# Optimization experiments

Hardware: AMD Instinct MI355X
Metric: run time of the kernel (lower is better)

## Reference

```python
import jax, jax.numpy as jnp
import numpy as np

D_MODEL = 2048
N_HEADS = 16
HEAD_DIM = 128
KV_RANK = 512


def setup_inputs() -> dict:
    key = jax.random.key(0)
    ks = jax.random.split(key, 6)
    s = lambda fan_in: 1.0 / np.sqrt(fan_in)
    return {
        "x": jax.random.normal(ks[0], (2, 2048, D_MODEL), dtype=jnp.float32),
        "Wq": jax.random.normal(ks[1], (D_MODEL, N_HEADS * HEAD_DIM), dtype=jnp.float32) * s(D_MODEL),
        "Wdown": jax.random.normal(ks[2], (D_MODEL, KV_RANK), dtype=jnp.float32) * s(D_MODEL),
        "Wk_up": jax.random.normal(ks[3], (KV_RANK, N_HEADS * HEAD_DIM), dtype=jnp.float32) * s(KV_RANK),
        "Wv_up": jax.random.normal(ks[4], (KV_RANK, N_HEADS * HEAD_DIM), dtype=jnp.float32) * s(KV_RANK),
        "Wo": jax.random.normal(ks[5], (N_HEADS * HEAD_DIM, D_MODEL), dtype=jnp.float32) * s(N_HEADS * HEAD_DIM),
    }


def reference(x, Wq, Wdown, Wk_up, Wv_up, Wo):
    B, T, _ = x.shape
    H, Dh = N_HEADS, HEAD_DIM
    # Q projection: (B,T,H,Dh) -> (B,H,T,Dh)
    Q = (x @ Wq).reshape(B, T, H, Dh).transpose(0, 2, 1, 3)
    # latent compression (this is the cached tensor)
    c = x @ Wdown  # (B, T, kv_lora_rank)
    # up-project latent to full K/V heads
    K = (c @ Wk_up).reshape(B, T, H, Dh).transpose(0, 2, 1, 3)
    V = (c @ Wv_up).reshape(B, T, H, Dh).transpose(0, 2, 1, 3)
    # causal SDPA (mask=None, past_kv=None -> is_causal=True), dropout=0
    scale = Dh ** (-0.5)
    scores = jnp.einsum("bhqd,bhkd->bhqk", Q, K) * scale
    causal = jnp.tril(jnp.ones((T, T), dtype=bool))
    scores = jnp.where(causal[None, None], scores, jnp.finfo(scores.dtype).min)
    attn = jax.nn.softmax(scores, axis=-1)
    out = jnp.einsum("bhqk,bhkd->bhqd", attn, V)
    out = out.transpose(0, 2, 1, 3).reshape(B, T, H * Dh)
    return out @ Wo, c
```

## Files before the change

### kernel.cpp

```cpp
#include <hip/hip_runtime.h>

typedef short bf16x8 __attribute__((ext_vector_type(8)));
typedef float f32x4 __attribute__((ext_vector_type(4)));

__device__ __forceinline__ void async16(const void* g, const void* l) {
  __builtin_amdgcn_global_load_lds(
      (const __attribute__((address_space(1))) unsigned int*)g,
      (__attribute__((address_space(3))) unsigned int*)(void*)(uintptr_t)l,
      16, 0, 0);
}

__device__ __forceinline__ unsigned short f2b(float f) {
  unsigned int u = __float_as_uint(f);
  u += 0x7fffu + ((u >> 16) & 1u);
  return (unsigned short)(u >> 16);
}

__global__ __launch_bounds__(256) void cast_f32_bf16(
    const float* __restrict__ in, unsigned short* __restrict__ out, int n) {
  int i = (blockIdx.x * 256 + threadIdx.x) * 4;
  if (i < n) {
    float4 v = *(const float4*)(in + i);
    ushort4 o;
    o.x = f2b(v.x); o.y = f2b(v.y); o.z = f2b(v.z); o.w = f2b(v.w);
    *(ushort4*)(out + i) = o;
  }
}

__global__ __launch_bounds__(256) void transpose_cast(
    const float* __restrict__ in, unsigned short* __restrict__ out,
    int K, int N) {
  __shared__ __align__(16) unsigned short tile[64][65];
  const int k0 = blockIdx.y * 64, n0 = blockIdx.x * 64;
  const int tid = threadIdx.x;
  const int r = tid >> 4, c4 = tid & 15;
#pragma unroll
  for (int p = 0; p < 4; ++p) {
    int row = p * 16 + r;
    float4 v = *(const float4*)(in + (size_t)(k0 + row) * N + n0 + c4 * 4);
    tile[c4 * 4 + 0][row] = f2b(v.x);
    tile[c4 * 4 + 1][row] = f2b(v.y);
    tile[c4 * 4 + 2][row] = f2b(v.z);
    tile[c4 * 4 + 3][row] = f2b(v.w);
  }
  __syncthreads();
#pragma unroll
  for (int p = 0; p < 4; ++p) {
    int nr = p * 16 + r;
    ushort4 o;
    o.x = tile[nr][c4 * 4 + 0];
    o.y = tile[nr][c4 * 4 + 1];
    o.z = tile[nr][c4 * 4 + 2];
    o.w = tile[nr][c4 * 4 + 3];
    *(ushort4*)(out + (size_t)(n0 + nr) * K + k0 + c4 * 4) = o;
  }
}

__global__ __launch_bounds__(256) void gemm_bt(
    const unsigned short* __restrict__ A, const unsigned short* __restrict__ BT,
    unsigned short* __restrict__ Cb, float* __restrict__ Cf, int M, int N, int K,
    float cscale) {
  __shared__ __align__(16) unsigned short sA[128 * 64];
  __shared__ __align__(16) unsigned short sB[128 * 64];
  const int tid = threadIdx.x;
  const int wave = tid >> 6, lane = tid & 63;
  const int quad = lane >> 4, cl = lane & 15;
  const int m0 = blockIdx.y * 128, n0 = blockIdx.x * 128;
  const int wm = (wave >> 1) * 64, wn = (wave & 1) * 64;
  (void)M;

  f32x4 acc[4][4] = {};

  const unsigned short* gA = A + (size_t)(m0 + wave * 32 + (lane >> 3)) * K + (lane & 7) * 8;
  const unsigned short* gB = BT + (size_t)(n0 + wave * 32 + (lane >> 3)) * K + (lane & 7) * 8;
  char* lA = (char*)sA + (wave * 32) * 128;
  char* lB = (char*)sB + (wave * 32) * 128;

  for (int kt = 0; kt < K; kt += 64) {
#pragma unroll
    for (int r = 0; r < 4; ++r) {
      async16(gA + (size_t)r * 8 * K + kt, lA + r * 8 * 128);
      async16(gB + (size_t)r * 8 * K + kt, lB + r * 8 * 128);
    }
    __syncthreads();
#pragma unroll
    for (int kk = 0; kk < 64; kk += 32) {
      bf16x8 af[4], bfr[4];
#pragma unroll
      for (int i = 0; i < 4; ++i)
        af[i] = *(const bf16x8*)((const char*)sA + (wm + i * 16 + cl) * 128 + kk * 2 + quad * 16);
#pragma unroll
      for (int j = 0; j < 4; ++j)
        bfr[j] = *(const bf16x8*)((const char*)sB + (wn + j * 16 + cl) * 128 + kk * 2 + quad * 16);
#pragma unroll
      for (int i = 0; i < 4; ++i)
#pragma unroll
        for (int j = 0; j < 4; ++j)
          acc[i][j] = __builtin_amdgcn_mfma_f32_16x16x32_bf16(af[i], bfr[j], acc[i][j], 0, 0, 0);
    }
    __syncthreads();
  }
#pragma unroll
  for (int i = 0; i < 4; ++i)
#pragma unroll
    for (int j = 0; j < 4; ++j)
#pragma unroll
      for (int r = 0; r < 4; ++r) {
        int row = m0 + wm + i * 16 + quad * 4 + r;
        int col = n0 + wn + j * 16 + cl;
        float v = acc[i][j][r];
        if (Cb) Cb[(size_t)row * N + col] = f2b(v * cscale);
        if (Cf) Cf[(size_t)row * N + col] = v;
      }
}

__global__ __launch_bounds__(256) void gemm_qc(
    const unsigned short* __restrict__ A, const unsigned short* __restrict__ BT,
    unsigned short* __restrict__ Qb, unsigned short* __restrict__ cb,
    float* __restrict__ cout, int K, float qscale) {
  __shared__ __align__(16) unsigned short sA[128 * 64];
  __shared__ __align__(16) unsigned short sB[128 * 64];
  const int tid = threadIdx.x;
  const int wave = tid >> 6, lane = tid & 63;
  const int quad = lane >> 4, cl = lane & 15;
  const int m0 = blockIdx.y * 128, n0 = blockIdx.x * 128;
  const int wm = (wave >> 1) * 64, wn = (wave & 1) * 64;

  f32x4 acc[4][4] = {};

  const unsigned short* gA = A + (size_t)(m0 + wave * 32 + (lane >> 3)) * K + (lane & 7) * 8;
  const unsigned short* gB = BT + (size_t)(n0 + wave * 32 + (lane >> 3)) * K + (lane & 7) * 8;
  char* lA = (char*)sA + (wave * 32) * 128;
  char* lB = (char*)sB + (wave * 32) * 128;

  for (int kt = 0; kt < K; kt += 64) {
#pragma unroll
    for (int r = 0; r < 4; ++r) {
      async16(gA + (size_t)r * 8 * K + kt, lA + r * 8 * 128);
      async16(gB + (size_t)r * 8 * K + kt, lB + r * 8 * 128);
    }
    __syncthreads();
#pragma unroll
    for (int kk = 0; kk < 64; kk += 32) {
      bf16x8 af[4], bfr[4];
#pragma unroll
      for (int i = 0; i < 4; ++i)
        af[i] = *(const bf16x8*)((const char*)sA + (wm + i * 16 + cl) * 128 + kk * 2 + quad * 16);
#pragma unroll
      for (int j = 0; j < 4; ++j)
        bfr[j] = *(const bf16x8*)((const char*)sB + (wn + j * 16 + cl) * 128 + kk * 2 + quad * 16);
#pragma unroll
      for (int i = 0; i < 4; ++i)
#pragma unroll
        for (int j = 0; j < 4; ++j)
          acc[i][j] = __builtin_amdgcn_mfma_f32_16x16x32_bf16(af[i], bfr[j], acc[i][j], 0, 0, 0);
    }
    __syncthreads();
  }
  const bool qreg = (n0 < 2048);
#pragma unroll
  for (int i = 0; i < 4; ++i)
#pragma unroll
    for (int j = 0; j < 4; ++j)
#pragma unroll
      for (int r = 0; r < 4; ++r) {
        int row = m0 + wm + i * 16 + quad * 4 + r;
        int col = n0 + wn + j * 16 + cl;
        float v = acc[i][j][r];
        if (qreg) {
          Qb[(size_t)row * 2048 + col] = f2b(v * qscale);
        } else {
          int c2 = col - 2048;
          cb[(size_t)row * 512 + c2] = f2b(v);
          cout[(size_t)row * 512 + c2] = v;
        }
      }
}

__global__ __launch_bounds__(256) void mla_attn(
    const unsigned short* __restrict__ Qm, const unsigned short* __restrict__ Km,
    const unsigned short* __restrict__ Vt, unsigned short* __restrict__ Om, int T) {
  const int ld = 2048;
  const int ldv = 4096;
  __shared__ __align__(16) unsigned short sK[2][64 * 128];
  __shared__ __align__(16) unsigned short sVT[128 * 64];
  __shared__ __align__(16) unsigned short sP[64 * 64];
  const int h = blockIdx.y, b = blockIdx.z;
  const int tid = threadIdx.x, wave = tid >> 6, lane = tid & 63;
  const int quad = lane >> 4, cl = lane & 15;
  const int nq = T / 64;

  for (int phase = 0; phase < 2; ++phase) {
    const int qt = phase ? (nq - 1 - blockIdx.x) : blockIdx.x;

    bf16x8 qf[4];
    {
      const unsigned short* Qg =
          Qm + (size_t)(b * T + qt * 64 + wave * 16 + cl) * ld + h * 128 + quad * 8;
#pragma unroll
      for (int kk = 0; kk < 4; ++kk)
        qf[kk] = *(const bf16x8*)(Qg + kk * 32);
    }

    float m_i[4], l_part[4];
    f32x4 acc_o[8] = {};
#pragma unroll
    for (int r = 0; r < 4; ++r) { m_i[r] = -1e30f; l_part[r] = 0.f; }

    const unsigned short* Kg0 = Km + (size_t)(b * T) * ld + h * 128;
    const unsigned short* Vg0 = Vt + (size_t)(h * 128) * ldv + (size_t)b * T;

#pragma unroll
    for (int r = 0; r < 4; ++r) {
      int c0 = r * 256 + wave * 64;
      int c = c0 + lane;
      int row = c >> 4, j = (c & 15) ^ (row & 7);
      async16(Kg0 + (size_t)row * ld + j * 8, (char*)sK[0] + c0 * 16);
    }
    __syncthreads();

    for (int kt = 0; kt <= qt; ++kt) {
      const int cur = kt & 1;
      const char* cK = (const char*)sK[cur];

      if (kt < qt) {
        const unsigned short* Kg = Kg0 + (size_t)(kt + 1) * 64 * ld;
        char* dK = (char*)sK[cur ^ 1];
#pragma unroll
        for (int r = 0; r < 4; ++r) {
          int c0 = r * 256 + wave * 64;
          int c = c0 + lane;
          int row = c >> 4, j = (c & 15) ^ (row & 7);
          async16(Kg + (size_t)row * ld + j * 8, dK + c0 * 16);
        }
      }
      {
        const unsigned short* Vg = Vg0 + kt * 64;
#pragma unroll
        for (int r = 0; r < 4; ++r) {
          int c0 = r * 256 + wave * 64;
          int c = c0 + lane;
          int d = c >> 3, jv = (c & 7) ^ (d & 7);
          async16(Vg + (size_t)d * ldv + jv * 8, (char*)sVT + c0 * 16);
        }
      }

      f32x4 s[4] = {};
      __builtin_amdgcn_s_setprio(1);
#pragma unroll
      for (int kk = 0; kk < 4; ++kk) {
#pragma unroll
        for (int j = 0; j < 4; ++j) {
          int t = j * 16 + cl;
          int jp = (kk * 4 + quad) ^ (t & 7);
          bf16x8 bk = *(const bf16x8*)(cK + (t * 16 + jp) * 16);
          s[j] = __builtin_amdgcn_mfma_f32_16x16x32_bf16(qf[kk], bk, s[j], 0, 0, 0);
        }
      }
      __builtin_amdgcn_s_setprio(0);

      const bool need_mask = (kt == qt);
#pragma unroll
      for (int r = 0; r < 4; ++r) {
        int q_l = wave * 16 + quad * 4 + r;
        float mxl = -1e30f;
#pragma unroll
        for (int j = 0; j < 4; ++j) {
          float v = s[j][r];
          if (need_mask) {
            int t_l = j * 16 + cl;
            if (t_l > q_l) v = -1e30f;
            s[j][r] = v;
          }
          mxl = fmaxf(mxl, v);
        }
        if (__any(mxl > m_i[r] + 6.f)) {
          float mx = mxl;
#pragma unroll
          for (int off = 1; off < 16; off <<= 1)
            mx = fmaxf(mx, __shfl_xor(mx, off));
          float m_new = fmaxf(m_i[r], mx);
          float alpha = exp2f(m_i[r] - m_new);
          m_i[r] = m_new;
          l_part[r] *= alpha;
#pragma unroll
          for (int jd = 0; jd < 8; ++jd)
            acc_o[jd][r] *= alpha;
        }
        float rs = 0.f;
#pragma unroll
        for (int j = 0; j < 4; ++j) {
          float p = exp2f(s[j][r] - m_i[r]);
          s[j][r] = p;
          rs += p;
        }
        l_part[r] += rs;
      }

#pragma unroll
      for (int j = 0; j < 4; ++j)
#pragma unroll
        for (int r = 0; r < 4; ++r) {
          int q = wave * 16 + quad * 4 + r;
          int swz = (q & 7) ^ (((q >> 3) & 1) << 1);
          int t = j * 16 + cl;
          int jp = (t >> 3) ^ swz;
          sP[(q * 8 + jp) * 8 + (t & 7)] = f2b(s[j][r]);
        }

      __syncthreads();

      __builtin_amdgcn_s_setprio(1);
#pragma unroll
      for (int kk2 = 0; kk2 < 2; ++kk2) {
        int q = wave * 16 + cl;
        int swz = (q & 7) ^ (((q >> 3) & 1) << 1);
        int jp = (kk2 * 4 + quad) ^ swz;
        bf16x8 ap = *(const bf16x8*)((const char*)sP + (q * 8 + jp) * 16);
#pragma unroll
        for (int jd = 0; jd < 8; ++jd) {
          int d = jd * 16 + cl;
          int jpv = (kk2 * 4 + quad) ^ (d & 7);
          bf16x8 bv = *(const bf16x8*)((const char*)sVT + (d * 8 + jpv) * 16);
          acc_o[jd] = __builtin_amdgcn_mfma_f32_16x16x32_bf16(ap, bv, acc_o[jd], 0, 0, 0);
        }
      }
      __builtin_amdgcn_s_setprio(0);

      __syncthreads();
    }

#pragma unroll
    for (int r = 0; r < 4; ++r) {
      float l = l_part[r];
#pragma unroll
      for (int off = 1; off < 16; off <<= 1)
        l += __shfl_xor(l, off);
      float inv = 1.f / l;
      int row = b * T + qt * 64 + wave * 16 + quad * 4 + r;
#pragma unroll
      for (int jd = 0; jd < 8; ++jd)
        Om[(size_t)row * ld + h * 128 + jd * 16 + cl] = f2b(acc_o[jd][r] * inv);
    }
  }
}

extern "C" void kernel_launch(void* const* d_in, const int* in_sizes, int n_in,
                              void* d_out, int out_size, void* d_ws, size_t ws_size,
                              hipStream_t stream) {
  (void)in_sizes; (void)n_in; (void)out_size; (void)ws_size;
  const int B = 2, T = 2048, Dm = 2048, H = 16, Dh = 128, R = 512;
  const int M = B * T;
  const float* x     = (const float*)d_in[0];
  const float* Wq    = (const float*)d_in[1];
  const float* Wdown = (const float*)d_in[2];
  const float* Wkup  = (const float*)d_in[3];
  const float* Wvup  = (const float*)d_in[4];
  const float* Wo    = (const float*)d_in[5];

  float* out  = (float*)d_out;
  float* cout = out + (size_t)M * Dm;

  unsigned short* ws  = (unsigned short*)d_ws;
  unsigned short* WqT = ws;
  unsigned short* WdT = WqT + (size_t)Dm * Dm;
  unsigned short* WoT = WdT + (size_t)R * Dm;
  unsigned short* WkT = WoT + (size_t)Dm * Dm;
  unsigned short* WvT = WkT + (size_t)Dm * R;
  unsigned short* xb  = WvT + (size_t)Dm * R;
  unsigned short* cb  = xb + (size_t)M * Dm;
  unsigned short* Qb  = cb + (size_t)M * R;
  unsigned short* Kb  = Qb + (size_t)M * Dm;
  unsigned short* VT  = Kb + (size_t)M * Dm;
  unsigned short* AO  = xb;

  const float qscale = 0.08838834764831845f * 1.4426950408889634f;

  cast_f32_bf16<<<(M * Dm) / 1024, 256, 0, stream>>>(x, xb, M * Dm);
  transpose_cast<<<dim3(32, 32), 256, 0, stream>>>(Wq, WqT, Dm, Dm);
  transpose_cast<<<dim3(8, 32), 256, 0, stream>>>(Wdown, WdT, Dm, R);
  transpose_cast<<<dim3(32, 32), 256, 0, stream>>>(Wo, WoT, Dm, Dm);
  transpose_cast<<<dim3(32, 8), 256, 0, stream>>>(Wkup, WkT, R, Dm);
  transpose_cast<<<dim3(32, 8), 256, 0, stream>>>(Wvup, WvT, R, Dm);

  gemm_qc<<<dim3(20, 32), 256, 0, stream>>>(xb, WqT, Qb, cb, cout, Dm, qscale);

  gemm_bt<<<dim3(Dm / 128, M / 128), 256, 0, stream>>>(cb, WkT, Kb, nullptr, M, Dm, R, 1.f);
  gemm_bt<<<dim3(M / 128, Dm / 128), 256, 0, stream>>>(WvT, cb, VT, nullptr, Dm, M, R, 1.f);

  mla_attn<<<dim3(T / 128, H, B), 256, 0, stream>>>(Qb, Kb, VT, AO, T);

  gemm_bt<<<dim3(Dm / 128, M / 128), 256, 0, stream>>>(AO, WoT, nullptr, out, M, Dm, Dm, 1.f);
  (void)Dh; (void)H;
}
```

Measured before the change: 398.7 us.

## Double-buffer LDS tiles and XOR-swizzle layout in projection GEMMs

Both projection GEMM kernels (gemm_bt and gemm_qc) now keep two LDS stages. The async global-to-LDS load for the next K tile is issued before the MFMA work on the current tile, so load latency can overlap compute. The LDS tile layout is also XOR-swizzled by row, on both the global-load side and the fragment-read side, to reduce bank conflicts on the 16-byte fragment reads. This doubles LDS usage per block to 64 KB, which may lower occupancy, and it still relies on the barrier at the end of each iteration to wait for the async loads.

```diff
diff --git a/kernel.cpp b/kernel.cpp
--- a/kernel.cpp
+++ b/kernel.cpp
@@ -60,8 +60,8 @@
     const unsigned short* __restrict__ A, const unsigned short* __restrict__ BT,
     unsigned short* __restrict__ Cb, float* __restrict__ Cf, int M, int N, int K,
     float cscale) {
-  __shared__ __align__(16) unsigned short sA[128 * 64];
-  __shared__ __align__(16) unsigned short sB[128 * 64];
+  __shared__ __align__(16) unsigned short sA[2][128 * 64];
+  __shared__ __align__(16) unsigned short sB[2][128 * 64];
   const int tid = threadIdx.x;
   const int wave = tid >> 6, lane = tid & 63;
   const int quad = lane >> 4, cl = lane & 15;
@@ -71,27 +71,47 @@
 
   f32x4 acc[4][4] = {};
 
-  const unsigned short* gA = A + (size_t)(m0 + wave * 32 + (lane >> 3)) * K + (lane & 7) * 8;
-  const unsigned short* gB = BT + (size_t)(n0 + wave * 32 + (lane >> 3)) * K + (lane & 7) * 8;
-  char* lA = (char*)sA + (wave * 32) * 128;
-  char* lB = (char*)sB + (wave * 32) * 128;
-
-  for (int kt = 0; kt < K; kt += 64) {
-#pragma unroll
-    for (int r = 0; r < 4; ++r) {
-      async16(gA + (size_t)r * 8 * K + kt, lA + r * 8 * 128);
-      async16(gB + (size_t)r * 8 * K + kt, lB + r * 8 * 128);
-    }
-    __syncthreads();
-#pragma unroll
-    for (int kk = 0; kk < 64; kk += 32) {
+  const int lr = lane >> 3;
+  const int lc = (lane & 7) ^ lr;
+  const unsigned short* gA = A + (size_t)(m0 + wave * 32 + lr) * K + lc * 8;
+  const unsigned short* gB = BT + (size_t)(n0 + wave * 32 + lr) * K + lc * 8;
+  const int nk = K >> 6;
+
+#pragma unroll
+  for (int r = 0; r < 4; ++r) {
+    async16(gA + (size_t)r * 8 * K, (char*)sA[0] + (wave * 32 + r * 8) * 128);
+    async16(gB + (size_t)r * 8 * K, (char*)sB[0] + (wave * 32 + r * 8) * 128);
+  }
+  __syncthreads();
+
+  for (int kt = 0; kt < nk; ++kt) {
+    const int cur = kt & 1;
+    if (kt + 1 < nk) {
+      const int k1 = (kt + 1) * 64;
+#pragma unroll
+      for (int r = 0; r < 4; ++r) {
+        async16(gA + (size_t)r * 8 * K + k1,
+                (char*)sA[cur ^ 1] + (wave * 32 + r * 8) * 128);
+        async16(gB + (size_t)r * 8 * K + k1,
+                (char*)sB[cur ^ 1] + (wave * 32 + r * 8) * 128);
+      }
+    }
+    const char* cA = (const char*)sA[cur];
+    const char* cB = (const char*)sB[cur];
+#pragma unroll
+    for (int kk = 0; kk < 2; ++kk) {
+      const int g = kk * 4 + quad;
       bf16x8 af[4], bfr[4];
 #pragma unroll
-      for (int i = 0; i < 4; ++i)
-        af[i] = *(const bf16x8*)((const char*)sA + (wm + i * 16 + cl) * 128 + kk * 2 + quad * 16);
-#pragma unroll
-      for (int j = 0; j < 4; ++j)
-        bfr[j] = *(const bf16x8*)((const char*)sB + (wn + j * 16 + cl) * 128 + kk * 2 + quad * 16);
+      for (int i = 0; i < 4; ++i) {
+        int row = wm + i * 16 + cl;
+        af[i] = *(const bf16x8*)(cA + row * 128 + (g ^ (cl & 7)) * 16);
+      }
+#pragma unroll
+      for (int j = 0; j < 4; ++j) {
+        int row = wn + j * 16 + cl;
+        bfr[j] = *(const bf16x8*)(cB + row * 128 + (g ^ (cl & 7)) * 16);
+      }
 #pragma unroll
       for (int i = 0; i < 4; ++i)
 #pragma unroll
@@ -118,8 +138,8 @@
     const unsigned short* __restrict__ A, const unsigned short* __restrict__ BT,
     unsigned short* __restrict__ Qb, unsigned short* __restrict__ cb,
     float* __restrict__ cout, int K, float qscale) {
-  __shared__ __align__(16) unsigned short sA[128 * 64];
-  __shared__ __align__(16) unsigned short sB[128 * 64];
+  __shared__ __align__(16) unsigned short sA[2][128 * 64];
+  __shared__ __align__(16) unsigned short sB[2][128 * 64];
   const int tid = threadIdx.x;
   const int wave = tid >> 6, lane = tid & 63;
   const int quad = lane >> 4, cl = lane & 15;
@@ -128,27 +148,47 @@
 
   f32x4 acc[4][4] = {};
 
-  const unsigned short* gA = A + (size_t)(m0 + wave * 32 + (lane >> 3)) * K + (lane & 7) * 8;
-  const unsigned short* gB = BT + (size_t)(n0 + wave * 32 + (lane >> 3)) * K + (lane & 7) * 8;
-  char* lA = (char*)sA + (wave * 32) * 128;
-  char* lB = (char*)sB + (wave * 32) * 128;
-
-  for (int kt = 0; kt < K; kt += 64) {
-#pragma unroll
-    for (int r = 0; r < 4; ++r) {
-      async16(gA + (size_t)r * 8 * K + kt, lA + r * 8 * 128);
-      async16(gB + (size_t)r * 8 * K + kt, lB + r * 8 * 128);
-    }
-    __syncthreads();
-#pragma unroll
-    for (int kk = 0; kk < 64; kk += 32) {
+  const int lr = lane >> 3;
+  const int lc = (lane & 7) ^ lr;
+  const unsigned short* gA = A + (size_t)(m0 + wave * 32 + lr) * K + lc * 8;
+  const unsigned short* gB = BT + (size_t)(n0 + wave * 32 + lr) * K + lc * 8;
+  const int nk = K >> 6;
+
+#pragma unroll
+  for (int r = 0; r < 4; ++r) {
+    async16(gA + (size_t)r * 8 * K, (char*)sA[0] + (wave * 32 + r * 8) * 128);
+    async16(gB + (size_t)r * 8 * K, (char*)sB[0] + (wave * 32 + r * 8) * 128);
+  }
+  __syncthreads();
+
+  for (int kt = 0; kt < nk; ++kt) {
+    const int cur = kt & 1;
+    if (kt + 1 < nk) {
+      const int k1 = (kt + 1) * 64;
+#pragma unroll
+      for (int r = 0; r < 4; ++r) {
+        async16(gA + (size_t)r * 8 * K + k1,
+                (char*)sA[cur ^ 1] + (wave * 32 + r * 8) * 128);
+        async16(gB + (size_t)r * 8 * K + k1,
+                (char*)sB[cur ^ 1] + (wave * 32 + r * 8) * 128);
+      }
+    }
+    const char* cA = (const char*)sA[cur];
+    const char* cB = (const char*)sB[cur];
+#pragma unroll
+    for (int kk = 0; kk < 2; ++kk) {
+      const int g = kk * 4 + quad;
       bf16x8 af[4], bfr[4];
 #pragma unroll
-      for (int i = 0; i < 4; ++i)
-        af[i] = *(const bf16x8*)((const char*)sA + (wm + i * 16 + cl) * 128 + kk * 2 + quad * 16);
-#pragma unroll
-      for (int j = 0; j < 4; ++j)
-        bfr[j] = *(const bf16x8*)((const char*)sB + (wn + j * 16 + cl) * 128 + kk * 2 + quad * 16);
+      for (int i = 0; i < 4; ++i) {
+        int row = wm + i * 16 + cl;
+        af[i] = *(const bf16x8*)(cA + row * 128 + (g ^ (cl & 7)) * 16);
+      }
+#pragma unroll
+      for (int j = 0; j < 4; ++j) {
+        int row = wn + j * 16 + cl;
+        bfr[j] = *(const bf16x8*)(cB + row * 128 + (g ^ (cl & 7)) * 16);
+      }
 #pragma unroll
       for (int i = 0; i < 4; ++i)
 #pragma unroll
```

Measured after the change: 368.2 us. -7.7%, faster.

## Double-buffer LDS tiles in projection GEMMs with K-step of 32

Applied to the files above, without the earlier changes.

Both GEMM kernels now split LDS into two 32-wide K buffers and issue async global-to-LDS loads for the next K slice while MFMAs run on the current one. This aims to hide global load latency that the single-buffer load-sync-compute loop exposed. In exchange there are twice as many loop iterations and barriers, and each wave loads half as much per step. The 64-byte LDS row stride may also cause bank conflicts on the fragment reads.

```diff
diff --git a/kernel.cpp b/kernel.cpp
--- a/kernel.cpp
+++ b/kernel.cpp
@@ -60,8 +60,8 @@
     const unsigned short* __restrict__ A, const unsigned short* __restrict__ BT,
     unsigned short* __restrict__ Cb, float* __restrict__ Cf, int M, int N, int K,
     float cscale) {
-  __shared__ __align__(16) unsigned short sA[128 * 64];
-  __shared__ __align__(16) unsigned short sB[128 * 64];
+  __shared__ __align__(16) unsigned short sA[2][128 * 32];
+  __shared__ __align__(16) unsigned short sB[2][128 * 32];
   const int tid = threadIdx.x;
   const int wave = tid >> 6, lane = tid & 63;
   const int quad = lane >> 4, cl = lane & 15;
@@ -71,33 +71,45 @@
 
   f32x4 acc[4][4] = {};
 
-  const unsigned short* gA = A + (size_t)(m0 + wave * 32 + (lane >> 3)) * K + (lane & 7) * 8;
-  const unsigned short* gB = BT + (size_t)(n0 + wave * 32 + (lane >> 3)) * K + (lane & 7) * 8;
-  char* lA = (char*)sA + (wave * 32) * 128;
-  char* lB = (char*)sB + (wave * 32) * 128;
-
-  for (int kt = 0; kt < K; kt += 64) {
-#pragma unroll
-    for (int r = 0; r < 4; ++r) {
-      async16(gA + (size_t)r * 8 * K + kt, lA + r * 8 * 128);
-      async16(gB + (size_t)r * 8 * K + kt, lB + r * 8 * 128);
-    }
-    __syncthreads();
-#pragma unroll
-    for (int kk = 0; kk < 64; kk += 32) {
-      bf16x8 af[4], bfr[4];
-#pragma unroll
-      for (int i = 0; i < 4; ++i)
-        af[i] = *(const bf16x8*)((const char*)sA + (wm + i * 16 + cl) * 128 + kk * 2 + quad * 16);
+  const int lr = lane >> 2;
+  const int lc = lane & 3;
+  const unsigned short* gA = A + (size_t)(m0 + wave * 32 + lr) * K + lc * 8;
+  const unsigned short* gB = BT + (size_t)(n0 + wave * 32 + lr) * K + lc * 8;
+  const int nk = K >> 5;
+
+#pragma unroll
+  for (int r = 0; r < 2; ++r) {
+    async16(gA + (size_t)r * 16 * K, (char*)sA[0] + (wave * 32 + r * 16) * 64);
+    async16(gB + (size_t)r * 16 * K, (char*)sB[0] + (wave * 32 + r * 16) * 64);
+  }
+  __syncthreads();
+
+  for (int kt = 0; kt < nk; ++kt) {
+    const int cur = kt & 1;
+    if (kt + 1 < nk) {
+      const int k1 = (kt + 1) * 32;
+#pragma unroll
+      for (int r = 0; r < 2; ++r) {
+        async16(gA + (size_t)r * 16 * K + k1,
+                (char*)sA[cur ^ 1] + (wave * 32 + r * 16) * 64);
+        async16(gB + (size_t)r * 16 * K + k1,
+                (char*)sB[cur ^ 1] + (wave * 32 + r * 16) * 64);
+      }
+    }
+    const char* cA = (const char*)sA[cur];
+    const char* cB = (const char*)sB[cur];
+    bf16x8 af[4], bfr[4];
+#pragma unroll
+    for (int i = 0; i < 4; ++i)
+      af[i] = *(const bf16x8*)(cA + (wm + i * 16 + cl) * 64 + quad * 16);
+#pragma unroll
+    for (int j = 0; j < 4; ++j)
+      bfr[j] = *(const bf16x8*)(cB + (wn + j * 16 + cl) * 64 + quad * 16);
+#pragma unroll
+    for (int i = 0; i < 4; ++i)
 #pragma unroll
       for (int j = 0; j < 4; ++j)
-        bfr[j] = *(const bf16x8*)((const char*)sB + (wn + j * 16 + cl) * 128 + kk * 2 + quad * 16);
-#pragma unroll
-      for (int i = 0; i < 4; ++i)
-#pragma unroll
-        for (int j = 0; j < 4; ++j)
-          acc[i][j] = __builtin_amdgcn_mfma_f32_16x16x32_bf16(af[i], bfr[j], acc[i][j], 0, 0, 0);
-    }
+        acc[i][j] = __builtin_amdgcn_mfma_f32_16x16x32_bf16(af[i], bfr[j], acc[i][j], 0, 0, 0);
     __syncthreads();
   }
 #pragma unroll
@@ -118,8 +130,8 @@
     const unsigned short* __restrict__ A, const unsigned short* __restrict__ BT,
     unsigned short* __restrict__ Qb, unsigned short* __restrict__ cb,
     float* __restrict__ cout, int K, float qscale) {
-  __shared__ __align__(16) unsigned short sA[128 * 64];
-  __shared__ __align__(16) unsigned short sB[128 * 64];
+  __shared__ __align__(16) unsigned short sA[2][128 * 32];
+  __shared__ __align__(16) unsigned short sB[2][128 * 32];
   const int tid = threadIdx.x;
   const int wave = tid >> 6, lane = tid & 63;
   const int quad = lane >> 4, cl = lane & 15;
@@ -128,33 +140,45 @@
 
   f32x4 acc[4][4] = {};
 
-  const unsigned short* gA = A + (size_t)(m0 + wave * 32 + (lane >> 3)) * K + (lane & 7) * 8;
-  const unsigned short* gB = BT + (size_t)(n0 + wave * 32 + (lane >> 3)) * K + (lane & 7) * 8;
-  char* lA = (char*)sA + (wave * 32) * 128;
-  char* lB = (char*)sB + (wave * 32) * 128;
-
-  for (int kt = 0; kt < K; kt += 64) {
-#pragma unroll
-    for (int r = 0; r < 4; ++r) {
-      async16(gA + (size_t)r * 8 * K + kt, lA + r * 8 * 128);
-      async16(gB + (size_t)r * 8 * K + kt, lB + r * 8 * 128);
-    }
-    __syncthreads();
-#pragma unroll
-    for (int kk = 0; kk < 64; kk += 32) {
-      bf16x8 af[4], bfr[4];
-#pragma unroll
-      for (int i = 0; i < 4; ++i)
-        af[i] = *(const bf16x8*)((const char*)sA + (wm + i * 16 + cl) * 128 + kk * 2 + quad * 16);
+  const int lr = lane >> 2;
+  const int lc = lane & 3;
+  const unsigned short* gA = A + (size_t)(m0 + wave * 32 + lr) * K + lc * 8;
+  const unsigned short* gB = BT + (size_t)(n0 + wave * 32 + lr) * K + lc * 8;
+  const int nk = K >> 5;
+
+#pragma unroll
+  for (int r = 0; r < 2; ++r) {
+    async16(gA + (size_t)r * 16 * K, (char*)sA[0] + (wave * 32 + r * 16) * 64);
+    async16(gB + (size_t)r * 16 * K, (char*)sB[0] + (wave * 32 + r * 16) * 64);
+  }
+  __syncthreads();
+
+  for (int kt = 0; kt < nk; ++kt) {
+    const int cur = kt & 1;
+    if (kt + 1 < nk) {
+      const int k1 = (kt + 1) * 32;
+#pragma unroll
+      for (int r = 0; r < 2; ++r) {
+        async16(gA + (size_t)r * 16 * K + k1,
+                (char*)sA[cur ^ 1] + (wave * 32 + r * 16) * 64);
+        async16(gB + (size_t)r * 16 * K + k1,
+                (char*)sB[cur ^ 1] + (wave * 32 + r * 16) * 64);
+      }
+    }
+    const char* cA = (const char*)sA[cur];
+    const char* cB = (const char*)sB[cur];
+    bf16x8 af[4], bfr[4];
+#pragma unroll
+    for (int i = 0; i < 4; ++i)
+      af[i] = *(const bf16x8*)(cA + (wm + i * 16 + cl) * 64 + quad * 16);
+#pragma unroll
+    for (int j = 0; j < 4; ++j)
+      bfr[j] = *(const bf16x8*)(cB + (wn + j * 16 + cl) * 64 + quad * 16);
+#pragma unroll
+    for (int i = 0; i < 4; ++i)
 #pragma unroll
       for (int j = 0; j < 4; ++j)
-        bfr[j] = *(const bf16x8*)((const char*)sB + (wn + j * 16 + cl) * 128 + kk * 2 + quad * 16);
-#pragma unroll
-      for (int i = 0; i < 4; ++i)
-#pragma unroll
-        for (int j = 0; j < 4; ++j)
-          acc[i][j] = __builtin_amdgcn_mfma_f32_16x16x32_bf16(af[i], bfr[j], acc[i][j], 0, 0, 0);
-    }
+        acc[i][j] = __builtin_amdgcn_mfma_f32_16x16x32_bf16(af[i], bfr[j], acc[i][j], 0, 0, 0);
     __syncthreads();
   }
   const bool qreg = (n0 < 2048);
```

Result: faster. 371.4 us (-6.9%).
